# Optimization experiments

Measured on AMD Instinct MI355X. Metric: run time of the kernel, lower is better.

## Reference

```python
import jax, jax.numpy as jnp
import numpy as np

N = 50000        # nodes
E = 800000       # edges (before self loops)
F_IN = 64        # num_features
DIM = 64         # num_hidden
C = 10           # num_classes
G = 256          # graphs in batch
NEG_SLOPE = 0.2


def setup_inputs() -> dict:
    key = jax.random.key(0)
    ks = jax.random.split(key, 20)
    def w(k, shape, fan_in):
        return jax.random.normal(k, shape, dtype=jnp.float32) / np.sqrt(fan_in)
    x = jax.random.normal(ks[0], (N, F_IN), dtype=jnp.float32)
    edge_index = jax.random.randint(ks[1], (2, E), 0, N, dtype=jnp.int64)
    batch = jnp.sort(jax.random.randint(ks[2], (N,), 0, G, dtype=jnp.int64))
    return {
        "x": x, "edge_index": edge_index, "batch": batch,
        "w1": w(ks[3], (F_IN, DIM), F_IN), "as1": w(ks[4], (DIM,), DIM), "ad1": w(ks[5], (DIM,), DIM), "b1": jnp.zeros((DIM,), jnp.float32),
        "w2": w(ks[6], (DIM, DIM), DIM),  "as2": w(ks[7], (DIM,), DIM), "ad2": w(ks[8], (DIM,), DIM), "b2": jnp.zeros((DIM,), jnp.float32),
        "w3": w(ks[9], (DIM, DIM), DIM),  "as3": w(ks[10], (DIM,), DIM), "ad3": w(ks[11], (DIM,), DIM), "b3": jnp.zeros((DIM,), jnp.float32),
        "fc1_w": w(ks[12], (DIM, DIM), DIM), "fc1_b": jnp.zeros((DIM,), jnp.float32),
        "fc2_w": w(ks[13], (DIM, C), DIM),   "fc2_b": jnp.zeros((C,), jnp.float32),
    }


def _gat_conv(x, src, dst, w, a_src, a_dst, b, n_nodes):
    # PyG GATConv, heads=1: h = x W; e_ij = LeakyReLU(a_src.h_j + a_dst.h_i);
    # alpha = segment-softmax over edges grouped by target i; out_i = sum_j alpha_ij h_j + b
    h = x @ w                                   # [N, DIM]
    alpha_s = h @ a_src                         # [N]
    alpha_d = h @ a_dst                         # [N]
    e = jax.nn.leaky_relu(alpha_s[src] + alpha_d[dst], NEG_SLOPE)  # [E']
    e_max = jax.ops.segment_max(e, dst, num_segments=n_nodes)
    e_exp = jnp.exp(e - e_max[dst])
    denom = jax.ops.segment_sum(e_exp, dst, num_segments=n_nodes)
    alpha = e_exp / (denom[dst] + 1e-16)        # [E']
    out = jax.ops.segment_sum(alpha[:, None] * h[src], dst, num_segments=n_nodes)
    return out + b


def _l2_normalize(x):
    nrm = jnp.linalg.norm(x, axis=1, keepdims=True)
    return x / jnp.maximum(nrm, 1e-12)


def reference(x, edge_index, batch, w1, as1, ad1, b1, w2, as2, ad2, b2,
              w3, as3, ad3, b3, fc1_w, fc1_b, fc2_w, fc2_b):
    n = x.shape[0]
    loops = jnp.arange(n, dtype=edge_index.dtype)
    src = jnp.concatenate([edge_index[0], loops])   # add_self_loops=True (PyG default)
    dst = jnp.concatenate([edge_index[1], loops])
    h = _gat_conv(x, src, dst, w1, as1, ad1, b1, n)
    h = jax.nn.relu(_l2_normalize(h))
    h = _gat_conv(h, src, dst, w2, as2, ad2, b2, n)
    h = jax.nn.relu(_l2_normalize(h))
    h = _gat_conv(h, src, dst, w3, as3, ad3, b3, n)
    h = jax.nn.relu(_l2_normalize(h))
    g = jax.ops.segment_sum(h, batch, num_segments=G)   # global_add_pool -> [G, DIM]
    g = jax.nn.relu(g @ fc1_w + fc1_b)
    logits = g @ fc2_w + fc2_b
    return jax.nn.log_softmax(logits, axis=-1)
```

## Files before the change

kernel.cpp:

```cpp
#include <hip/hip_runtime.h>
#include <hip/hip_bf16.h>
#include <math.h>

#define DIM 64
#define GNUM 256
#define CNUM 10

__device__ __forceinline__ unsigned bfpack(float a, float b) {
    unsigned ua = __builtin_bit_cast(unsigned, a);
    unsigned ub = __builtin_bit_cast(unsigned, b);
    ua += 0x7fffu + ((ua >> 16) & 1u);
    ub += 0x7fffu + ((ub >> 16) & 1u);
    return (ua >> 16) | (ub & 0xffff0000u);
}
__device__ __forceinline__ float bfs(unsigned short u) { return __builtin_bit_cast(float, (unsigned)u << 16); }

typedef float floatx2 __attribute__((ext_vector_type(2)));
__device__ __forceinline__ unsigned fp8x4_enc(float a, float b, float c, float d) {
    int w = __builtin_amdgcn_cvt_pk_fp8_f32(a, b, 0, false);
    w = __builtin_amdgcn_cvt_pk_fp8_f32(c, d, w, true);
    return (unsigned)w;
}
__device__ __forceinline__ void fp8dec8(uint2 h, float* f) {
    floatx2 p0 = __builtin_amdgcn_cvt_pk_f32_fp8((int)h.x, false);
    floatx2 p1 = __builtin_amdgcn_cvt_pk_f32_fp8((int)h.x, true);
    floatx2 p2 = __builtin_amdgcn_cvt_pk_f32_fp8((int)h.y, false);
    floatx2 p3 = __builtin_amdgcn_cvt_pk_f32_fp8((int)h.y, true);
    f[0] = p0[0]; f[1] = p0[1]; f[2] = p1[0]; f[3] = p1[1];
    f[4] = p2[0]; f[5] = p2[1]; f[6] = p3[0]; f[7] = p3[1];
}

__global__ void deg_rank_kernel(const int* __restrict__ ei, int E, int N,
                                int* __restrict__ deg, int* __restrict__ rank) {
    int i = blockIdx.x * blockDim.x + threadIdx.x;
    int EP = E + N;
    if (i >= EP) return;
    int d = (i < E) ? ei[E + i] : (i - E);
    rank[i] = atomicAdd(&deg[d], 1);
}

__global__ __launch_bounds__(256) void scan_misc(const int* __restrict__ deg, int* __restrict__ part, int n, int nb,
                                                 const int* __restrict__ batch, int N,
                                                 int* __restrict__ gstart) {
    int bid = blockIdx.x;
    if (bid < nb) {
        __shared__ int ws[4];
        int i = bid * 256 + threadIdx.x;
        int v = (i < n) ? deg[i] : 0;
        #pragma unroll
        for (int d = 32; d >= 1; d >>= 1) v += __shfl_xor(v, d);
        if ((threadIdx.x & 63) == 0) ws[threadIdx.x >> 6] = v;
        __syncthreads();
        if (threadIdx.x == 0) part[bid] = ws[0] + ws[1] + ws[2] + ws[3];
    } else {
        for (int g = threadIdx.x; g <= GNUM; g += 256) {
            int lo = 0, hi = N;
            while (lo < hi) { int mid = (lo + hi) >> 1; if (batch[mid] < g) lo = mid + 1; else hi = mid; }
            gstart[g] = lo;
        }
    }
}

__global__ __launch_bounds__(256) void scan_down(const int* __restrict__ deg, const int* __restrict__ part,
                                                 int* __restrict__ offs, int n) {
    __shared__ int ws[4];
    __shared__ int base_s;
    int tid = threadIdx.x, lane = tid & 63, wid = tid >> 6;
    int pv = (tid < (int)blockIdx.x) ? part[tid] : 0;
    #pragma unroll
    for (int d = 32; d >= 1; d >>= 1) pv += __shfl_xor(pv, d);
    if (lane == 0) ws[wid] = pv;
    __syncthreads();
    if (tid == 0) base_s = ws[0] + ws[1] + ws[2] + ws[3];
    __syncthreads();
    int i = blockIdx.x * 256 + tid;
    int v = (i < n) ? deg[i] : 0;
    int x = v;
    #pragma unroll
    for (int d = 1; d < 64; d <<= 1) { int t = __shfl_up(x, d); if (lane >= d) x += t; }
    if (lane == 63) ws[wid] = x;
    __syncthreads();
    int add = base_s;
    for (int w = 0; w < wid; ++w) add += ws[w];
    if (i < n) offs[i] = add + x - v;
    if (i == n - 1) offs[n] = add + x;
}

__device__ __forceinline__ void gat_gather4(const unsigned* __restrict__ hb,
                                            const int2* __restrict__ lsw,
                                            int ls, int deg, int fg,
                                            float& a0, float& a1, float& a2, float& a3,
                                            float& a4, float& a5, float& a6, float& a7,
                                            float& sw) {
    for (int eb = 0; eb < deg; eb += 4) {
        int t = ls + eb;
        int2 eA = lsw[t], eB = lsw[t + 1], eC = lsw[t + 2], eD = lsw[t + 3];
        float wA = __builtin_bit_cast(float, eA.y);
        float wB = (eb + 1 < deg) ? __builtin_bit_cast(float, eB.y) : 0.f;
        float wC = (eb + 2 < deg) ? __builtin_bit_cast(float, eC.y) : 0.f;
        float wD = (eb + 3 < deg) ? __builtin_bit_cast(float, eD.y) : 0.f;
        const uint2 hA = *(const uint2*)(hb + ((size_t)eA.x << 4) + (fg << 1));
        const uint2 hB = *(const uint2*)(hb + ((size_t)eB.x << 4) + (fg << 1));
        const uint2 hC = *(const uint2*)(hb + ((size_t)eC.x << 4) + (fg << 1));
        const uint2 hD = *(const uint2*)(hb + ((size_t)eD.x << 4) + (fg << 1));
        float fA[8], fB[8], fC[8], fD[8];
        fp8dec8(hA, fA); fp8dec8(hB, fB); fp8dec8(hC, fC); fp8dec8(hD, fD);
        sw += wA + wB + wC + wD;
        a0 += wA * fA[0] + wB * fB[0] + wC * fC[0] + wD * fD[0];
        a1 += wA * fA[1] + wB * fB[1] + wC * fC[1] + wD * fD[1];
        a2 += wA * fA[2] + wB * fB[2] + wC * fC[2] + wD * fD[2];
        a3 += wA * fA[3] + wB * fB[3] + wC * fC[3] + wD * fD[3];
        a4 += wA * fA[4] + wB * fB[4] + wC * fC[4] + wD * fD[4];
        a5 += wA * fA[5] + wB * fB[5] + wC * fC[5] + wD * fD[5];
        a6 += wA * fA[6] + wB * fB[6] + wC * fC[6] + wD * fD[6];
        a7 += wA * fA[7] + wB * fB[7] + wC * fC[7] + wD * fD[7];
    }
}

#define XSTR 68
__device__ __forceinline__ void mm_core_512(const float* __restrict__ xT, const float* __restrict__ Ws,
                                            const float* __restrict__ a_s, const float* __restrict__ a_d,
                                            unsigned* __restrict__ hbn, float* __restrict__ asn,
                                            float* __restrict__ adn, int base, int N) {
    int tid = threadIdx.x;
    int tx = tid & 15, ty = tid >> 4;
    int c0 = tx << 2, r0 = ty << 1;
    float acc[2][4] = {{0.f}};
    #pragma unroll 8
    for (int k = 0; k < DIM; ++k) {
        float2 xv = *(const float2*)(xT + k * XSTR + r0);
        float4 wv = *(const float4*)(Ws + k * DIM + c0);
        acc[0][0] += xv.x * wv.x; acc[0][1] += xv.x * wv.y; acc[0][2] += xv.x * wv.z; acc[0][3] += xv.x * wv.w;
        acc[1][0] += xv.y * wv.x; acc[1][1] += xv.y * wv.y; acc[1][2] += xv.y * wv.z; acc[1][3] += xv.y * wv.w;
    }
    float4 av = *(const float4*)(a_s + c0);
    float4 dv = *(const float4*)(a_d + c0);
    #pragma unroll
    for (int ri = 0; ri < 2; ++ri) {
        int grow = base + r0 + ri;
        float s1 = acc[ri][0] * av.x + acc[ri][1] * av.y + acc[ri][2] * av.z + acc[ri][3] * av.w;
        float s2 = acc[ri][0] * dv.x + acc[ri][1] * dv.y + acc[ri][2] * dv.z + acc[ri][3] * dv.w;
        #pragma unroll
        for (int d = 1; d <= 8; d <<= 1) { s1 += __shfl_xor(s1, d); s2 += __shfl_xor(s2, d); }
        if (grow < N) {
            hbn[((size_t)grow << 4) + tx] = fp8x4_enc(acc[ri][0], acc[ri][1], acc[ri][2], acc[ri][3]);
            if (tx == 0) { asn[grow] = s1; adn[grow] = s2; }
        }
    }
}

__global__ __launch_bounds__(512) void mm_fill(const float* __restrict__ in, const float* __restrict__ W,
                                               const float* __restrict__ a_s, const float* __restrict__ a_d,
                                               unsigned* __restrict__ hb, float* __restrict__ as_,
                                               float* __restrict__ ad_, int N, int nbt,
                                               const int* __restrict__ ei, const int* __restrict__ rank, int E,
                                               const int* __restrict__ offs, int2* __restrict__ csr_sd) {
    int bid = blockIdx.x;
    if (bid < nbt) {
        __shared__ float Ws[DIM * DIM];
        __shared__ float xT[XSTR * DIM];
        int tid = threadIdx.x;
        int base = bid * 64;

        const float4* W4 = (const float4*)W;
        float4* Ws4 = (float4*)Ws;
        Ws4[tid] = W4[tid];
        Ws4[tid + 512] = W4[tid + 512];

        {
            int row = tid >> 3;
            int kb = (tid & 7) << 3;
            int grow = base + row;
            int crow = grow < N ? grow : N - 1;
            const float4* xr = (const float4*)(in + ((size_t)crow << 6) + kb);
            float4 v0 = xr[0], v1 = xr[1];
            xT[(kb + 0) * XSTR + row] = v0.x;  xT[(kb + 1) * XSTR + row] = v0.y;
            xT[(kb + 2) * XSTR + row] = v0.z;  xT[(kb + 3) * XSTR + row] = v0.w;
            xT[(kb + 4) * XSTR + row] = v1.x;  xT[(kb + 5) * XSTR + row] = v1.y;
            xT[(kb + 6) * XSTR + row] = v1.z;  xT[(kb + 7) * XSTR + row] = v1.w;
        }
        __syncthreads();
        mm_core_512(xT, Ws, a_s, a_d, hb, as_, ad_, base, N);
    } else {
        int i = (bid - nbt) * 512 + threadIdx.x;
        int EP = E + N;
        if (i >= EP) return;
        int s, d;
        if (i < E) { s = ei[i]; d = ei[E + i]; } else { s = i - E; d = i - E; }
        csr_sd[offs[d] + rank[i]] = make_int2(s, d);
    }
}

#define FUS_NPB 64
#define FUS_CAP 2560
__global__ __launch_bounds__(512) void agg_mm(const unsigned* __restrict__ hbp,
                                              const int2* __restrict__ csr_sd,
                                              const float* __restrict__ asp,
                                              const float* __restrict__ adp,
                                              const int* __restrict__ offs,
                                              const float* __restrict__ bias,
                                              const float* __restrict__ W,
                                              const float* __restrict__ a_s,
                                              const float* __restrict__ a_d,
                                              unsigned* __restrict__ hbn,
                                              float* __restrict__ asn,
                                              float* __restrict__ adn, int N) {
    __shared__ int soffs[FUS_NPB + 1];
    __shared__ float adl[FUS_NPB];
    __shared__ int2 lsw[FUS_CAP + 4];
    __shared__ float xT[XSTR * DIM];
    float* Ws = (float*)lsw;

    int tid = threadIdx.x;
    int base = blockIdx.x * FUS_NPB;
    if (tid <= FUS_NPB) {
        int n = base + tid;
        soffs[tid] = offs[n < N ? n : N];
    }
    if (tid < FUS_NPB) {
        int n = base + tid;
        adl[tid] = (n < N) ? adp[n] : 0.f;
    }
    __syncthreads();
    int estart = soffs[0];
    int nE = soffs[FUS_NPB] - estart;
    bool inLds = (nE <= FUS_CAP);
    if (inLds) {
        for (int i = tid; i < nE; i += 512) {
            int2 sd = csr_sd[estart + i];
            float e = asp[sd.x] + adl[sd.y - base];
            e = (e > 0.f) ? e : 0.2f * e;
            lsw[i] = make_int2(sd.x, __builtin_bit_cast(int, expf(e)));
        }
        if (tid < 4) lsw[nE + tid] = make_int2(0, 0);
    }
    __syncthreads();

    int li = tid >> 3, fg = tid & 7;
    int node = base + li;
    int ls = soffs[li] - estart;
    int deg = soffs[li + 1] - soffs[li];

    float a0 = 0.f, a1 = 0.f, a2 = 0.f, a3 = 0.f;
    float a4 = 0.f, a5 = 0.f, a6 = 0.f, a7 = 0.f, sw = 0.f;
    if (inLds) {
        gat_gather4(hbp, lsw, ls, deg, fg, a0, a1, a2, a3, a4, a5, a6, a7, sw);
    } else {
        float adi = adl[li];
        for (int eb = 0; eb < deg; eb += 4) {
            int t = estart + ls + eb;
            float wv[4]; int sv[4];
            #pragma unroll
            for (int k = 0; k < 4; ++k) {
                int2 sd = (eb + k < deg) ? csr_sd[t + k] : make_int2(0, 0);
                int s = sd.x; s = s < 0 ? 0 : (s >= N ? N - 1 : s);
                float e = asp[s] + adi;
                e = (e > 0.f) ? e : 0.2f * e;
                wv[k] = (eb + k < deg) ? expf(e) : 0.f;
                sv[k] = s;
            }
            #pragma unroll
            for (int k = 0; k < 4; ++k) {
                const uint2 hv = *(const uint2*)(hbp + ((size_t)sv[k] << 4) + (fg << 1));
                float fv[8];
                fp8dec8(hv, fv);
                sw += wv[k];
                a0 += wv[k] * fv[0]; a1 += wv[k] * fv[1];
                a2 += wv[k] * fv[2]; a3 += wv[k] * fv[3];
                a4 += wv[k] * fv[4]; a5 += wv[k] * fv[5];
                a6 += wv[k] * fv[6]; a7 += wv[k] * fv[7];
            }
        }
    }

    float inv = 1.f / (sw + 1e-16f);
    const float4 b0 = *(const float4*)(bias + (fg << 3));
    const float4 b1 = *(const float4*)(bias + (fg << 3) + 4);
    float o0 = a0 * inv + b0.x, o1 = a1 * inv + b0.y, o2 = a2 * inv + b0.z, o3 = a3 * inv + b0.w;
    float o4 = a4 * inv + b1.x, o5 = a5 * inv + b1.y, o6 = a6 * inv + b1.z, o7 = a7 * inv + b1.w;
    float n2 = o0 * o0 + o1 * o1 + o2 * o2 + o3 * o3 + o4 * o4 + o5 * o5 + o6 * o6 + o7 * o7;
    #pragma unroll
    for (int d = 1; d <= 4; d <<= 1) n2 += __shfl_xor(n2, d);
    float innrm = 1.f / fmaxf(sqrtf(n2), 1e-12f);
    if (node >= N) innrm = 0.f;
    int kb = fg << 3;
    xT[(kb + 0) * XSTR + li] = fmaxf(o0 * innrm, 0.f);
    xT[(kb + 1) * XSTR + li] = fmaxf(o1 * innrm, 0.f);
    xT[(kb + 2) * XSTR + li] = fmaxf(o2 * innrm, 0.f);
    xT[(kb + 3) * XSTR + li] = fmaxf(o3 * innrm, 0.f);
    xT[(kb + 4) * XSTR + li] = fmaxf(o4 * innrm, 0.f);
    xT[(kb + 5) * XSTR + li] = fmaxf(o5 * innrm, 0.f);
    xT[(kb + 6) * XSTR + li] = fmaxf(o6 * innrm, 0.f);
    xT[(kb + 7) * XSTR + li] = fmaxf(o7 * innrm, 0.f);
    __syncthreads();

    const float4* W4 = (const float4*)W;
    float4* Ws4 = (float4*)Ws;
    Ws4[tid] = W4[tid];
    Ws4[tid + 512] = W4[tid + 512];
    __syncthreads();
    mm_core_512(xT, Ws, a_s, a_d, hbn, asn, adn, base, N);
}

#define AGG_NPB 64
#define AGG_CAP 2560
__global__ __launch_bounds__(512) void gat_agg(const unsigned* __restrict__ hb,
                                               const int2* __restrict__ csr_sd,
                                               const float* __restrict__ as_,
                                               const float* __restrict__ ad_,
                                               const int* __restrict__ offs,
                                               const float* __restrict__ bias,
                                               unsigned* __restrict__ outb, int N) {
    __shared__ int soffs[AGG_NPB + 1];
    __shared__ float adl[AGG_NPB];
    __shared__ int2 lsw[AGG_CAP + 4];
    int tid = threadIdx.x;
    int base = blockIdx.x * AGG_NPB;
    if (tid <= AGG_NPB) {
        int n = base + tid;
        soffs[tid] = offs[n < N ? n : N];
    }
    if (tid < AGG_NPB) {
        int n = base + tid;
        adl[tid] = (n < N) ? ad_[n] : 0.f;
    }
    __syncthreads();
    int estart = soffs[0];
    int nE = soffs[AGG_NPB] - estart;
    bool inLds = (nE <= AGG_CAP);
    if (inLds) {
        for (int i = tid; i < nE; i += 512) {
            int2 sd = csr_sd[estart + i];
            float e = as_[sd.x] + adl[sd.y - base];
            e = (e > 0.f) ? e : 0.2f * e;
            lsw[i] = make_int2(sd.x, __builtin_bit_cast(int, expf(e)));
        }
        if (tid < 4) lsw[nE + tid] = make_int2(0, 0);
    }
    __syncthreads();

    int li = tid >> 3, fg = tid & 7;
    int node = base + li;
    int ls = soffs[li] - estart;
    int deg = soffs[li + 1] - soffs[li];

    float a0 = 0.f, a1 = 0.f, a2 = 0.f, a3 = 0.f;
    float a4 = 0.f, a5 = 0.f, a6 = 0.f, a7 = 0.f, sw = 0.f;
    if (inLds) {
        gat_gather4(hb, lsw, ls, deg, fg, a0, a1, a2, a3, a4, a5, a6, a7, sw);
    } else {
        float adi = (node < N) ? ad_[node] : 0.f;
        for (int eb = 0; eb < deg; eb += 4) {
            int t = estart + ls + eb;
            float wv[4]; int sv[4];
            #pragma unroll
            for (int k = 0; k < 4; ++k) {
                int2 sd = (eb + k < deg) ? csr_sd[t + k] : make_int2(0, 0);
                int s = sd.x; s = s < 0 ? 0 : (s >= N ? N - 1 : s);
                float e = as_[s] + adi;
                e = (e > 0.f) ? e : 0.2f * e;
                wv[k] = (eb + k < deg) ? expf(e) : 0.f;
                sv[k] = s;
            }
            #pragma unroll
            for (int k = 0; k < 4; ++k) {
                const uint2 hv = *(const uint2*)(hb + ((size_t)sv[k] << 4) + (fg << 1));
                float fv[8];
                fp8dec8(hv, fv);
                sw += wv[k];
                a0 += wv[k] * fv[0]; a1 += wv[k] * fv[1];
                a2 += wv[k] * fv[2]; a3 += wv[k] * fv[3];
                a4 += wv[k] * fv[4]; a5 += wv[k] * fv[5];
                a6 += wv[k] * fv[6]; a7 += wv[k] * fv[7];
            }
        }
    }

    float inv = 1.f / (sw + 1e-16f);
    const float4 b0 = *(const float4*)(bias + (fg << 3));
    const float4 b1 = *(const float4*)(bias + (fg << 3) + 4);
    float o0 = a0 * inv + b0.x, o1 = a1 * inv + b0.y, o2 = a2 * inv + b0.z, o3 = a3 * inv + b0.w;
    float o4 = a4 * inv + b1.x, o5 = a5 * inv + b1.y, o6 = a6 * inv + b1.z, o7 = a7 * inv + b1.w;
    float n2 = o0 * o0 + o1 * o1 + o2 * o2 + o3 * o3 + o4 * o4 + o5 * o5 + o6 * o6 + o7 * o7;
    #pragma unroll
    for (int d = 1; d <= 4; d <<= 1) n2 += __shfl_xor(n2, d);
    float innrm = 1.f / fmaxf(sqrtf(n2), 1e-12f);
    if (node < N) {
        uint4 o;
        o.x = bfpack(fmaxf(o0 * innrm, 0.f), fmaxf(o1 * innrm, 0.f));
        o.y = bfpack(fmaxf(o2 * innrm, 0.f), fmaxf(o3 * innrm, 0.f));
        o.z = bfpack(fmaxf(o4 * innrm, 0.f), fmaxf(o5 * innrm, 0.f));
        o.w = bfpack(fmaxf(o6 * innrm, 0.f), fmaxf(o7 * innrm, 0.f));
        *(uint4*)(outb + ((size_t)node << 5) + (fg << 2)) = o;
    }
}

__global__ __launch_bounds__(256) void pool_mlp(const unsigned short* __restrict__ hb, const int* __restrict__ gstart,
                                                const float* __restrict__ fc1w, const float* __restrict__ fc1b,
                                                const float* __restrict__ fc2w, const float* __restrict__ fc2b,
                                                float* __restrict__ out) {
    __shared__ float W1[DIM * DIM];
    __shared__ float red[4 * DIM];
    __shared__ float tbuf[DIM];
    __shared__ float obuf[CNUM];
    int tid = threadIdx.x, lane = tid & 63, wv = tid >> 6;
    int gid = blockIdx.x;

    const float4* W4 = (const float4*)fc1w;
    float4* W1s = (float4*)W1;
    #pragma unroll
    for (int i = 0; i < 4; ++i) W1s[tid + 256 * i] = W4[tid + 256 * i];

    int s = gstart[gid], e = gstart[gid + 1];
    float acc = 0.f;
    for (int i = s + wv; i < e; i += 4) acc += bfs(hb[((size_t)i << 6) + lane]);
    red[wv * DIM + lane] = acc;
    __syncthreads();

    if (wv == 0) {
        float g = red[lane] + red[DIM + lane] + red[2 * DIM + lane] + red[3 * DIM + lane];
        float t = fc1b[lane];
        #pragma unroll
        for (int k = 0; k < DIM; ++k) t += __shfl(g, k) * W1[k * DIM + lane];
        t = fmaxf(t, 0.f);
        tbuf[lane] = t;
        float o = 0.f;
        if (lane < CNUM) {
            o = fc2b[lane];
            #pragma unroll
            for (int k = 0; k < DIM; ++k) o += tbuf[k] * fc2w[k * CNUM + lane];
            obuf[lane] = o;
        }
        if (lane < CNUM) {
            float mx = obuf[0];
            #pragma unroll
            for (int k = 1; k < CNUM; ++k) mx = fmaxf(mx, obuf[k]);
            float ssum = 0.f;
            #pragma unroll
            for (int k = 0; k < CNUM; ++k) ssum += expf(obuf[k] - mx);
            out[gid * CNUM + lane] = o - mx - logf(ssum);
        }
    }
}

static inline size_t align256(size_t x) { return (x + 255) & ~size_t(255); }

extern "C" void kernel_launch(void* const* d_in, const int* in_sizes, int n_in,
                              void* d_out, int out_size, void* d_ws, size_t ws_size,
                              hipStream_t stream) {
    const float* x     = (const float*)d_in[0];
    const int*   ei    = (const int*)d_in[1];
    const int*   batch = (const int*)d_in[2];
    const float* w1  = (const float*)d_in[3];
    const float* as1 = (const float*)d_in[4];
    const float* ad1 = (const float*)d_in[5];
    const float* b1  = (const float*)d_in[6];
    const float* w2  = (const float*)d_in[7];
    const float* as2 = (const float*)d_in[8];
    const float* ad2 = (const float*)d_in[9];
    const float* b2  = (const float*)d_in[10];
    const float* w3  = (const float*)d_in[11];
    const float* as3 = (const float*)d_in[12];
    const float* ad3 = (const float*)d_in[13];
    const float* b3  = (const float*)d_in[14];
    const float* fc1w = (const float*)d_in[15];
    const float* fc1b = (const float*)d_in[16];
    const float* fc2w = (const float*)d_in[17];
    const float* fc2b = (const float*)d_in[18];
    float* out = (float*)d_out;

    int N  = in_sizes[0] / DIM;
    int E  = in_sizes[1] / 2;
    int EP = E + N;
    int nb = (N + 255) / 256;

    char* p = (char*)d_ws;
    unsigned* hbA = (unsigned*)p; p += align256(sizeof(unsigned) * (size_t)N * (DIM / 4));
    unsigned* hbB = (unsigned*)p; p += align256(sizeof(unsigned) * (size_t)N * (DIM / 4));
    unsigned* oAb = (unsigned*)p; p += align256(sizeof(unsigned) * (size_t)N * (DIM / 2));
    float* asA  = (float*)p; p += align256(sizeof(float) * (size_t)N);
    float* adA  = (float*)p; p += align256(sizeof(float) * (size_t)N);
    float* asB  = (float*)p; p += align256(sizeof(float) * (size_t)N);
    float* adB  = (float*)p; p += align256(sizeof(float) * (size_t)N);
    int*   deg  = (int*)p;   p += align256(sizeof(int) * (size_t)N);
    int*   offs = (int*)p;   p += align256(sizeof(int) * (size_t)(N + 1));
    int*   rank = (int*)p;   p += align256(sizeof(int) * (size_t)EP);
    int2*  csr_sd = (int2*)p; p += align256(sizeof(int2) * (size_t)EP);
    int*   part = (int*)p;   p += align256(sizeof(int) * (size_t)nb);
    int*   gst  = (int*)p;   p += align256(sizeof(int) * (size_t)(GNUM + 1));

    int nfb  = (N + FUS_NPB - 1) / FUS_NPB;
    int nblk = (N + AGG_NPB - 1) / AGG_NPB;
    int nbt = (N + 63) / 64;
    int epBlocks = (EP + 511) / 512;

    hipMemsetAsync(deg, 0, sizeof(int) * (size_t)N, stream);
    deg_rank_kernel<<<(EP + 255) / 256, 256, 0, stream>>>(ei, E, N, deg, rank);
    scan_misc<<<nb + 1, 256, 0, stream>>>(deg, part, N, nb, batch, N, gst);
    scan_down<<<nb, 256, 0, stream>>>(deg, part, offs, N);

    mm_fill<<<nbt + epBlocks, 512, 0, stream>>>(x, w1, as1, ad1, hbA, asA, adA, N, nbt,
                                                ei, rank, E, offs, csr_sd);
    agg_mm<<<nfb, 512, 0, stream>>>(hbA, csr_sd, asA, adA, offs, b1, w2, as2, ad2,
                                    hbB, asB, adB, N);
    agg_mm<<<nfb, 512, 0, stream>>>(hbB, csr_sd, asB, adB, offs, b2, w3, as3, ad3,
                                    hbA, asA, adA, N);
    gat_agg<<<nblk, 512, 0, stream>>>(hbA, csr_sd, asA, adA, offs, b3, oAb, N);

    pool_mlp<<<GNUM, 256, 0, stream>>>((const unsigned short*)oAb, gst, fc1w, fc1b, fc2w, fc2b, out);
}
```

Baseline: 248.2 us.

## Compute source attention scores on the fly from gathered features, shrink CSR to src-only

Stops precomputing per-node source attention scores (alpha_s). Each edge's score is now recomputed inside the gather as a dot product of the fp8-decoded neighbor features with a_src, reduced across the 8-lane feature group with shuffles. This removes the extra random gather of as_[src] and lets the CSR hold only source indices (int instead of int2), which halves edge-list traffic and doubles LDS edge capacity. In exchange it adds per-edge FMAs and shuffles, and the scores now come from fp8-quantized features rather than fp32 values, which changes accuracy.

```diff
diff --git a/kernel.cpp b/kernel.cpp
--- a/kernel.cpp
+++ b/kernel.cpp
@@ -86,42 +86,60 @@
     if (i == n - 1) offs[n] = add + x;
 }
 
-__device__ __forceinline__ void gat_gather4(const unsigned* __restrict__ hb,
-                                            const int2* __restrict__ lsw,
-                                            int ls, int deg, int fg,
-                                            float& a0, float& a1, float& a2, float& a3,
-                                            float& a4, float& a5, float& a6, float& a7,
-                                            float& sw) {
+__device__ __forceinline__ void gat_gather_fa(const unsigned* __restrict__ hb,
+                                              const int* __restrict__ lsrc,
+                                              int ls, int deg, int fg,
+                                              const float* __restrict__ av, float adi,
+                                              float& a0, float& a1, float& a2, float& a3,
+                                              float& a4, float& a5, float& a6, float& a7,
+                                              float& sw) {
     for (int eb = 0; eb < deg; eb += 4) {
         int t = ls + eb;
-        int2 eA = lsw[t], eB = lsw[t + 1], eC = lsw[t + 2], eD = lsw[t + 3];
-        float wA = __builtin_bit_cast(float, eA.y);
-        float wB = (eb + 1 < deg) ? __builtin_bit_cast(float, eB.y) : 0.f;
-        float wC = (eb + 2 < deg) ? __builtin_bit_cast(float, eC.y) : 0.f;
-        float wD = (eb + 3 < deg) ? __builtin_bit_cast(float, eD.y) : 0.f;
-        const uint2 hA = *(const uint2*)(hb + ((size_t)eA.x << 4) + (fg << 1));
-        const uint2 hB = *(const uint2*)(hb + ((size_t)eB.x << 4) + (fg << 1));
-        const uint2 hC = *(const uint2*)(hb + ((size_t)eC.x << 4) + (fg << 1));
-        const uint2 hD = *(const uint2*)(hb + ((size_t)eD.x << 4) + (fg << 1));
-        float fA[8], fB[8], fC[8], fD[8];
-        fp8dec8(hA, fA); fp8dec8(hB, fB); fp8dec8(hC, fC); fp8dec8(hD, fD);
-        sw += wA + wB + wC + wD;
-        a0 += wA * fA[0] + wB * fB[0] + wC * fC[0] + wD * fD[0];
-        a1 += wA * fA[1] + wB * fB[1] + wC * fC[1] + wD * fD[1];
-        a2 += wA * fA[2] + wB * fB[2] + wC * fC[2] + wD * fD[2];
-        a3 += wA * fA[3] + wB * fB[3] + wC * fC[3] + wD * fD[3];
-        a4 += wA * fA[4] + wB * fB[4] + wC * fC[4] + wD * fD[4];
-        a5 += wA * fA[5] + wB * fB[5] + wC * fC[5] + wD * fD[5];
-        a6 += wA * fA[6] + wB * fB[6] + wC * fC[6] + wD * fD[6];
-        a7 += wA * fA[7] + wB * fB[7] + wC * fC[7] + wD * fD[7];
+        int s0 = lsrc[t], s1 = lsrc[t + 1], s2 = lsrc[t + 2], s3 = lsrc[t + 3];
+        const uint2 h0 = *(const uint2*)(hb + ((size_t)s0 << 4) + (fg << 1));
+        const uint2 h1 = *(const uint2*)(hb + ((size_t)s1 << 4) + (fg << 1));
+        const uint2 h2 = *(const uint2*)(hb + ((size_t)s2 << 4) + (fg << 1));
+        const uint2 h3 = *(const uint2*)(hb + ((size_t)s3 << 4) + (fg << 1));
+        float f0[8], f1[8], f2[8], f3[8];
+        fp8dec8(h0, f0); fp8dec8(h1, f1); fp8dec8(h2, f2); fp8dec8(h3, f3);
+        float d0 = 0.f, d1 = 0.f, d2 = 0.f, d3 = 0.f;
+        #pragma unroll
+        for (int j = 0; j < 8; ++j) {
+            d0 += f0[j] * av[j]; d1 += f1[j] * av[j];
+            d2 += f2[j] * av[j]; d3 += f3[j] * av[j];
+        }
+        #pragma unroll
+        for (int d = 1; d <= 4; d <<= 1) {
+            d0 += __shfl_xor(d0, d); d1 += __shfl_xor(d1, d);
+            d2 += __shfl_xor(d2, d); d3 += __shfl_xor(d3, d);
+        }
+        float e0 = d0 + adi, e1 = d1 + adi, e2 = d2 + adi, e3 = d3 + adi;
+        e0 = (e0 > 0.f) ? e0 : 0.2f * e0;
+        e1 = (e1 > 0.f) ? e1 : 0.2f * e1;
+        e2 = (e2 > 0.f) ? e2 : 0.2f * e2;
+        e3 = (e3 > 0.f) ? e3 : 0.2f * e3;
+        int rem = deg - eb;
+        float w0 = expf(e0);
+        float w1 = (rem > 1) ? expf(e1) : 0.f;
+        float w2 = (rem > 2) ? expf(e2) : 0.f;
+        float w3 = (rem > 3) ? expf(e3) : 0.f;
+        sw += (w0 + w1) + (w2 + w3);
+        a0 += w0 * f0[0] + w1 * f1[0] + w2 * f2[0] + w3 * f3[0];
+        a1 += w0 * f0[1] + w1 * f1[1] + w2 * f2[1] + w3 * f3[1];
+        a2 += w0 * f0[2] + w1 * f1[2] + w2 * f2[2] + w3 * f3[2];
+        a3 += w0 * f0[3] + w1 * f1[3] + w2 * f2[3] + w3 * f3[3];
+        a4 += w0 * f0[4] + w1 * f1[4] + w2 * f2[4] + w3 * f3[4];
+        a5 += w0 * f0[5] + w1 * f1[5] + w2 * f2[5] + w3 * f3[5];
+        a6 += w0 * f0[6] + w1 * f1[6] + w2 * f2[6] + w3 * f3[6];
+        a7 += w0 * f0[7] + w1 * f1[7] + w2 * f2[7] + w3 * f3[7];
     }
 }
 
 #define XSTR 68
 __device__ __forceinline__ void mm_core_512(const float* __restrict__ xT, const float* __restrict__ Ws,
-                                            const float* __restrict__ a_s, const float* __restrict__ a_d,
-                                            unsigned* __restrict__ hbn, float* __restrict__ asn,
-                                            float* __restrict__ adn, int base, int N) {
+                                            const float* __restrict__ adv,
+                                            unsigned* __restrict__ hbn, float* __restrict__ adn,
+                                            int base, int N) {
     int tid = threadIdx.x;
     int tx = tid & 15, ty = tid >> 4;
     int c0 = tx << 2, r0 = ty << 1;
@@ -133,28 +151,26 @@
         acc[0][0] += xv.x * wv.x; acc[0][1] += xv.x * wv.y; acc[0][2] += xv.x * wv.z; acc[0][3] += xv.x * wv.w;
         acc[1][0] += xv.y * wv.x; acc[1][1] += xv.y * wv.y; acc[1][2] += xv.y * wv.z; acc[1][3] += xv.y * wv.w;
     }
-    float4 av = *(const float4*)(a_s + c0);
-    float4 dv = *(const float4*)(a_d + c0);
+    float4 dv = *(const float4*)(adv + c0);
     #pragma unroll
     for (int ri = 0; ri < 2; ++ri) {
         int grow = base + r0 + ri;
-        float s1 = acc[ri][0] * av.x + acc[ri][1] * av.y + acc[ri][2] * av.z + acc[ri][3] * av.w;
         float s2 = acc[ri][0] * dv.x + acc[ri][1] * dv.y + acc[ri][2] * dv.z + acc[ri][3] * dv.w;
         #pragma unroll
-        for (int d = 1; d <= 8; d <<= 1) { s1 += __shfl_xor(s1, d); s2 += __shfl_xor(s2, d); }
+        for (int d = 1; d <= 8; d <<= 1) s2 += __shfl_xor(s2, d);
         if (grow < N) {
             hbn[((size_t)grow << 4) + tx] = fp8x4_enc(acc[ri][0], acc[ri][1], acc[ri][2], acc[ri][3]);
-            if (tx == 0) { asn[grow] = s1; adn[grow] = s2; }
+            if (tx == 0) adn[grow] = s2;
         }
     }
 }
 
 __global__ __launch_bounds__(512) void mm_fill(const float* __restrict__ in, const float* __restrict__ W,
-                                               const float* __restrict__ a_s, const float* __restrict__ a_d,
-                                               unsigned* __restrict__ hb, float* __restrict__ as_,
-                                               float* __restrict__ ad_, int N, int nbt,
+                                               const float* __restrict__ adv,
+                                               unsigned* __restrict__ hb, float* __restrict__ ad_,
+                                               int N, int nbt,
                                                const int* __restrict__ ei, const int* __restrict__ rank, int E,
-                                               const int* __restrict__ offs, int2* __restrict__ csr_sd) {
+                                               const int* __restrict__ offs, int* __restrict__ csr) {
     int bid = blockIdx.x;
     if (bid < nbt) {
         __shared__ float Ws[DIM * DIM];
@@ -180,36 +196,34 @@
             xT[(kb + 6) * XSTR + row] = v1.z;  xT[(kb + 7) * XSTR + row] = v1.w;
         }
         __syncthreads();
-        mm_core_512(xT, Ws, a_s, a_d, hb, as_, ad_, base, N);
+        mm_core_512(xT, Ws, adv, hb, ad_, base, N);
     } else {
         int i = (bid - nbt) * 512 + threadIdx.x;
         int EP = E + N;
         if (i >= EP) return;
         int s, d;
         if (i < E) { s = ei[i]; d = ei[E + i]; } else { s = i - E; d = i - E; }
-        csr_sd[offs[d] + rank[i]] = make_int2(s, d);
+        csr[offs[d] + rank[i]] = s;
     }
 }
 
 #define FUS_NPB 64
-#define FUS_CAP 2560
+#define FUS_CAP 5120
 __global__ __launch_bounds__(512) void agg_mm(const unsigned* __restrict__ hbp,
-                                              const int2* __restrict__ csr_sd,
-                                              const float* __restrict__ asp,
+                                              const int* __restrict__ csr,
                                               const float* __restrict__ adp,
                                               const int* __restrict__ offs,
+                                              const float* __restrict__ asv,
                                               const float* __restrict__ bias,
                                               const float* __restrict__ W,
-                                              const float* __restrict__ a_s,
-                                              const float* __restrict__ a_d,
+                                              const float* __restrict__ adv,
                                               unsigned* __restrict__ hbn,
-                                              float* __restrict__ asn,
                                               float* __restrict__ adn, int N) {
     __shared__ int soffs[FUS_NPB + 1];
     __shared__ float adl[FUS_NPB];
-    __shared__ int2 lsw[FUS_CAP + 4];
+    __shared__ __attribute__((aligned(16))) int lsrc[FUS_CAP + 4];
     __shared__ float xT[XSTR * DIM];
-    float* Ws = (float*)lsw;
+    float* Ws = (float*)lsrc;
 
     int tid = threadIdx.x;
     int base = blockIdx.x * FUS_NPB;
@@ -226,13 +240,8 @@
     int nE = soffs[FUS_NPB] - estart;
     bool inLds = (nE <= FUS_CAP);
     if (inLds) {
-        for (int i = tid; i < nE; i += 512) {
-            int2 sd = csr_sd[estart + i];
-            float e = asp[sd.x] + adl[sd.y - base];
-            e = (e > 0.f) ? e : 0.2f * e;
-            lsw[i] = make_int2(sd.x, __builtin_bit_cast(int, expf(e)));
-        }
-        if (tid < 4) lsw[nE + tid] = make_int2(0, 0);
+        for (int i = tid; i < nE; i += 512) lsrc[i] = csr[estart + i];
+        if (tid < 4) lsrc[nE + tid] = 0;
     }
     __syncthreads();
 
@@ -240,36 +249,60 @@
     int node = base + li;
     int ls = soffs[li] - estart;
     int deg = soffs[li + 1] - soffs[li];
+    float adi = adl[li];
+
+    float av[8];
+    *(float4*)&av[0] = *(const float4*)(asv + (fg << 3));
+    *(float4*)&av[4] = *(const float4*)(asv + (fg << 3) + 4);
 
     float a0 = 0.f, a1 = 0.f, a2 = 0.f, a3 = 0.f;
     float a4 = 0.f, a5 = 0.f, a6 = 0.f, a7 = 0.f, sw = 0.f;
     if (inLds) {
-        gat_gather4(hbp, lsw, ls, deg, fg, a0, a1, a2, a3, a4, a5, a6, a7, sw);
+        gat_gather_fa(hbp, lsrc, ls, deg, fg, av, adi, a0, a1, a2, a3, a4, a5, a6, a7, sw);
     } else {
-        float adi = adl[li];
         for (int eb = 0; eb < deg; eb += 4) {
             int t = estart + ls + eb;
-            float wv[4]; int sv[4];
+            int sv[4];
             #pragma unroll
             for (int k = 0; k < 4; ++k) {
-                int2 sd = (eb + k < deg) ? csr_sd[t + k] : make_int2(0, 0);
-                int s = sd.x; s = s < 0 ? 0 : (s >= N ? N - 1 : s);
-                float e = asp[s] + adi;
-                e = (e > 0.f) ? e : 0.2f * e;
-                wv[k] = (eb + k < deg) ? expf(e) : 0.f;
-                sv[k] = s;
+                int s = (eb + k < deg) ? csr[t + k] : 0;
+                sv[k] = s < 0 ? 0 : (s >= N ? N - 1 : s);
             }
-            #pragma unroll
-            for (int k = 0; k < 4; ++k) {
-                const uint2 hv = *(const uint2*)(hbp + ((size_t)sv[k] << 4) + (fg << 1));
-                float fv[8];
-                fp8dec8(hv, fv);
-                sw += wv[k];
-                a0 += wv[k] * fv[0]; a1 += wv[k] * fv[1];
-                a2 += wv[k] * fv[2]; a3 += wv[k] * fv[3];
-                a4 += wv[k] * fv[4]; a5 += wv[k] * fv[5];
-                a6 += wv[k] * fv[6]; a7 += wv[k] * fv[7];
+            float f0[8], f1[8], f2[8], f3[8];
+            fp8dec8(*(const uint2*)(hbp + ((size_t)sv[0] << 4) + (fg << 1)), f0);
+            fp8dec8(*(const uint2*)(hbp + ((size_t)sv[1] << 4) + (fg << 1)), f1);
+            fp8dec8(*(const uint2*)(hbp + ((size_t)sv[2] << 4) + (fg << 1)), f2);
+            fp8dec8(*(const uint2*)(hbp + ((size_t)sv[3] << 4) + (fg << 1)), f3);
+            float d0 = 0.f, d1 = 0.f, d2 = 0.f, d3 = 0.f;
+            #pragma unroll
+            for (int j = 0; j < 8; ++j) {
+                d0 += f0[j] * av[j]; d1 += f1[j] * av[j];
+                d2 += f2[j] * av[j]; d3 += f3[j] * av[j];
             }
+            #pragma unroll
+            for (int d = 1; d <= 4; d <<= 1) {
+                d0 += __shfl_xor(d0, d); d1 += __shfl_xor(d1, d);
+                d2 += __shfl_xor(d2, d); d3 += __shfl_xor(d3, d);
+            }
+            float e0 = d0 + adi, e1 = d1 + adi, e2 = d2 + adi, e3 = d3 + adi;
+            e0 = (e0 > 0.f) ? e0 : 0.2f * e0;
+            e1 = (e1 > 0.f) ? e1 : 0.2f * e1;
+            e2 = (e2 > 0.f) ? e2 : 0.2f * e2;
+            e3 = (e3 > 0.f) ? e3 : 0.2f * e3;
+            int rem = deg - eb;
+            float w0 = expf(e0);
+            float w1 = (rem > 1) ? expf(e1) : 0.f;
+            float w2 = (rem > 2) ? expf(e2) : 0.f;
+            float w3 = (rem > 3) ? expf(e3) : 0.f;
+            sw += (w0 + w1) + (w2 + w3);
+            a0 += w0 * f0[0] + w1 * f1[0] + w2 * f2[0] + w3 * f3[0];
+            a1 += w0 * f0[1] + w1 * f1[1] + w2 * f2[1] + w3 * f3[1];
+            a2 += w0 * f0[2] + w1 * f1[2] + w2 * f2[2] + w3 * f3[2];
+            a3 += w0 * f0[3] + w1 * f1[3] + w2 * f2[3] + w3 * f3[3];
+            a4 += w0 * f0[4] + w1 * f1[4] + w2 * f2[4] + w3 * f3[4];
+            a5 += w0 * f0[5] + w1 * f1[5] + w2 * f2[5] + w3 * f3[5];
+            a6 += w0 * f0[6] + w1 * f1[6] + w2 * f2[6] + w3 * f3[6];
+            a7 += w0 * f0[7] + w1 * f1[7] + w2 * f2[7] + w3 * f3[7];
         }
     }
 
@@ -299,21 +332,21 @@
     Ws4[tid] = W4[tid];
     Ws4[tid + 512] = W4[tid + 512];
     __syncthreads();
-    mm_core_512(xT, Ws, a_s, a_d, hbn, asn, adn, base, N);
+    mm_core_512(xT, Ws, adv, hbn, adn, base, N);
 }
 
 #define AGG_NPB 64
-#define AGG_CAP 2560
+#define AGG_CAP 5120
 __global__ __launch_bounds__(512) void gat_agg(const unsigned* __restrict__ hb,
-                                               const int2* __restrict__ csr_sd,
-                                               const float* __restrict__ as_,
-                                               const float* __restrict__ ad_,
+                                               const int* __restrict__ csr,
+                                               const float* __restrict__ adp,
                                                const int* __restrict__ offs,
+                                               const float* __restrict__ asv,
                                                const float* __restrict__ bias,
                                                unsigned* __restrict__ outb, int N) {
     __shared__ int soffs[AGG_NPB + 1];
     __shared__ float adl[AGG_NPB];
-    __shared__ int2 lsw[AGG_CAP + 4];
+    __shared__ __attribute__((aligned(16))) int lsrc[AGG_CAP + 4];
     int tid = threadIdx.x;
     int base = blockIdx.x * AGG_NPB;
     if (tid <= AGG_NPB) {
@@ -322,20 +355,15 @@
     }
     if (tid < AGG_NPB) {
         int n = base + tid;
-        adl[tid] = (n < N) ? ad_[n] : 0.f;
+        adl[tid] = (n < N) ? adp[n] : 0.f;
     }
     __syncthreads();
     int estart = soffs[0];
     int nE = soffs[AGG_NPB] - estart;
     bool inLds = (nE <= AGG_CAP);
     if (inLds) {
-        for (int i = tid; i < nE; i += 512) {
-            int2 sd = csr_sd[estart + i];
-            float e = as_[sd.x] + adl[sd.y - base];
-            e = (e > 0.f) ? e : 0.2f * e;
-            lsw[i] = make_int2(sd.x, __builtin_bit_cast(int, expf(e)));
-        }
-        if (tid < 4) lsw[nE + tid] = make_int2(0, 0);
+        for (int i = tid; i < nE; i += 512) lsrc[i] = csr[estart + i];
+        if (tid < 4) lsrc[nE + tid] = 0;
     }
     __syncthreads();
 
@@ -343,36 +371,60 @@
     int node = base + li;
     int ls = soffs[li] - estart;
     int deg = soffs[li + 1] - soffs[li];
+    float adi = adl[li];
+
+    float av[8];
+    *(float4*)&av[0] = *(const float4*)(asv + (fg << 3));
+    *(float4*)&av[4] = *(const float4*)(asv + (fg << 3) + 4);
 
     float a0 = 0.f, a1 = 0.f, a2 = 0.f, a3 = 0.f;
     float a4 = 0.f, a5 = 0.f, a6 = 0.f, a7 = 0.f, sw = 0.f;
     if (inLds) {
-        gat_gather4(hb, lsw, ls, deg, fg, a0, a1, a2, a3, a4, a5, a6, a7, sw);
+        gat_gather_fa(hb, lsrc, ls, deg, fg, av, adi, a0, a1, a2, a3, a4, a5, a6, a7, sw);
     } else {
-        float adi = (node < N) ? ad_[node] : 0.f;
         for (int eb = 0; eb < deg; eb += 4) {
             int t = estart + ls + eb;
-            float wv[4]; int sv[4];
+            int sv[4];
             #pragma unroll
             for (int k = 0; k < 4; ++k) {
-                int2 sd = (eb + k < deg) ? csr_sd[t + k] : make_int2(0, 0);
-                int s = sd.x; s = s < 0 ? 0 : (s >= N ? N - 1 : s);
-                float e = as_[s] + adi;
-                e = (e > 0.f) ? e : 0.2f * e;
-                wv[k] = (eb + k < deg) ? expf(e) : 0.f;
-                sv[k] = s;
+                int s = (eb + k < deg) ? csr[t + k] : 0;
+                sv[k] = s < 0 ? 0 : (s >= N ? N - 1 : s);
             }
-            #pragma unroll
-            for (int k = 0; k < 4; ++k) {
-                const uint2 hv = *(const uint2*)(hb + ((size_t)sv[k] << 4) + (fg << 1));
-                float fv[8];
-                fp8dec8(hv, fv);
-                sw += wv[k];
-                a0 += wv[k] * fv[0]; a1 += wv[k] * fv[1];
-                a2 += wv[k] * fv[2]; a3 += wv[k] * fv[3];
-                a4 += wv[k] * fv[4]; a5 += wv[k] * fv[5];
-                a6 += wv[k] * fv[6]; a7 += wv[k] * fv[7];
+            float f0[8], f1[8], f2[8], f3[8];
+            fp8dec8(*(const uint2*)(hb + ((size_t)sv[0] << 4) + (fg << 1)), f0);
+            fp8dec8(*(const uint2*)(hb + ((size_t)sv[1] << 4) + (fg << 1)), f1);
+            fp8dec8(*(const uint2*)(hb + ((size_t)sv[2] << 4) + (fg << 1)), f2);
+            fp8dec8(*(const uint2*)(hb + ((size_t)sv[3] << 4) + (fg << 1)), f3);
+            float d0 = 0.f, d1 = 0.f, d2 = 0.f, d3 = 0.f;
+            #pragma unroll
+            for (int j = 0; j < 8; ++j) {
+                d0 += f0[j] * av[j]; d1 += f1[j] * av[j];
+                d2 += f2[j] * av[j]; d3 += f3[j] * av[j];
             }
+            #pragma unroll
+            for (int d = 1; d <= 4; d <<= 1) {
+                d0 += __shfl_xor(d0, d); d1 += __shfl_xor(d1, d);
+                d2 += __shfl_xor(d2, d); d3 += __shfl_xor(d3, d);
+            }
+            float e0 = d0 + adi, e1 = d1 + adi, e2 = d2 + adi, e3 = d3 + adi;
+            e0 = (e0 > 0.f) ? e0 : 0.2f * e0;
+            e1 = (e1 > 0.f) ? e1 : 0.2f * e1;
+            e2 = (e2 > 0.f) ? e2 : 0.2f * e2;
+            e3 = (e3 > 0.f) ? e3 : 0.2f * e3;
+            int rem = deg - eb;
+            float w0 = expf(e0);
+            float w1 = (rem > 1) ? expf(e1) : 0.f;
+            float w2 = (rem > 2) ? expf(e2) : 0.f;
+            float w3 = (rem > 3) ? expf(e3) : 0.f;
+            sw += (w0 + w1) + (w2 + w3);
+            a0 += w0 * f0[0] + w1 * f1[0] + w2 * f2[0] + w3 * f3[0];
+            a1 += w0 * f0[1] + w1 * f1[1] + w2 * f2[1] + w3 * f3[1];
+            a2 += w0 * f0[2] + w1 * f1[2] + w2 * f2[2] + w3 * f3[2];
+            a3 += w0 * f0[3] + w1 * f1[3] + w2 * f2[3] + w3 * f3[3];
+            a4 += w0 * f0[4] + w1 * f1[4] + w2 * f2[4] + w3 * f3[4];
+            a5 += w0 * f0[5] + w1 * f1[5] + w2 * f2[5] + w3 * f3[5];
+            a6 += w0 * f0[6] + w1 * f1[6] + w2 * f2[6] + w3 * f3[6];
+            a7 += w0 * f0[7] + w1 * f1[7] + w2 * f2[7] + w3 * f3[7];
         }
     }
 
@@ -478,14 +530,12 @@
     unsigned* hbA = (unsigned*)p; p += align256(sizeof(unsigned) * (size_t)N * (DIM / 4));
     unsigned* hbB = (unsigned*)p; p += align256(sizeof(unsigned) * (size_t)N * (DIM / 4));
     unsigned* oAb = (unsigned*)p; p += align256(sizeof(unsigned) * (size_t)N * (DIM / 2));
-    float* asA  = (float*)p; p += align256(sizeof(float) * (size_t)N);
     float* adA  = (float*)p; p += align256(sizeof(float) * (size_t)N);
-    float* asB  = (float*)p; p += align256(sizeof(float) * (size_t)N);
     float* adB  = (float*)p; p += align256(sizeof(float) * (size_t)N);
     int*   deg  = (int*)p;   p += align256(sizeof(int) * (size_t)N);
     int*   offs = (int*)p;   p += align256(sizeof(int) * (size_t)(N + 1));
     int*   rank = (int*)p;   p += align256(sizeof(int) * (size_t)EP);
-    int2*  csr_sd = (int2*)p; p += align256(sizeof(int2) * (size_t)EP);
+    int*   csr  = (int*)p;   p += align256(sizeof(int) * (size_t)(EP + 8));
     int*   part = (int*)p;   p += align256(sizeof(int) * (size_t)nb);
     int*   gst  = (int*)p;   p += align256(sizeof(int) * (size_t)(GNUM + 1));
 
@@ -499,13 +549,11 @@
     scan_misc<<<nb + 1, 256, 0, stream>>>(deg, part, N, nb, batch, N, gst);
     scan_down<<<nb, 256, 0, stream>>>(deg, part, offs, N);
 
-    mm_fill<<<nbt + epBlocks, 512, 0, stream>>>(x, w1, as1, ad1, hbA, asA, adA, N, nbt,
-                                                ei, rank, E, offs, csr_sd);
-    agg_mm<<<nfb, 512, 0, stream>>>(hbA, csr_sd, asA, adA, offs, b1, w2, as2, ad2,
-                                    hbB, asB, adB, N);
-    agg_mm<<<nfb, 512, 0, stream>>>(hbB, csr_sd, asB, adB, offs, b2, w3, as3, ad3,
-                                    hbA, asA, adA, N);
-    gat_agg<<<nblk, 512, 0, stream>>>(hbA, csr_sd, asA, adA, offs, b3, oAb, N);
+    mm_fill<<<nbt + epBlocks, 512, 0, stream>>>(x, w1, ad1, hbA, adA, N, nbt,
+                                                ei, rank, E, offs, csr);
+    agg_mm<<<nfb, 512, 0, stream>>>(hbA, csr, adA, offs, as1, b1, w2, ad2, hbB, adB, N);
+    agg_mm<<<nfb, 512, 0, stream>>>(hbB, csr, adB, offs, as2, b2, w3, ad3, hbA, adA, N);
+    gat_agg<<<nblk, 512, 0, stream>>>(hbA, csr, adA, offs, as3, b3, oAb, N);
 
     pool_mlp<<<GNUM, 256, 0, stream>>>((const unsigned short*)oAb, gst, fc1w, fc1b, fc2w, fc2b, out);
 }
```

Measured after the change: 270.6 us. +9.1%, slower.
